# Kernel optimization log

Measured on AMD Instinct MI355X. Metric: run time of the kernel, lower is better.

Reference implementation:

```python
import jax, jax.numpy as jnp
import numpy as np

B, L, H = 32, 2048, 1024

def setup_inputs() -> dict:
    key = jax.random.key(0)
    ks = jax.random.split(key, 10)
    scale = 1.0 / np.sqrt(H)
    return {
        "query": jax.random.normal(ks[0], (B, 1, H), dtype=jnp.float32),
        "key": jax.random.normal(ks[1], (B, L, H), dtype=jnp.float32),
        "value": jax.random.normal(ks[2], (B, L, H), dtype=jnp.float32),
        "mask": jax.random.randint(ks[3], (B, L), 0, 2, dtype=jnp.int32),
        "Wa_w": jax.random.normal(ks[4], (H, H), dtype=jnp.float32) * scale,
        "Wa_b": jax.random.normal(ks[5], (H,), dtype=jnp.float32) * scale,
        "Ua_w": jax.random.normal(ks[6], (H, H), dtype=jnp.float32) * scale,
        "Ua_b": jax.random.normal(ks[7], (H,), dtype=jnp.float32) * scale,
        "va_w": jax.random.normal(ks[8], (1, H), dtype=jnp.float32) * scale,
        "va_b": jax.random.normal(ks[9], (1,), dtype=jnp.float32) * scale,
    }

def reference(query, key, value, mask, Wa_w, Wa_b, Ua_w, Ua_b, va_w, va_b):
    # query: [B,1,H] -> squeeze, project with Wa
    q = jnp.einsum('bh,oh->bo', query[:, 0, :], Wa_w) + Wa_b          # [B,H]
    # key: [B,L,H] projected with Ua
    k = jnp.einsum('blh,oh->blo', key, Ua_w) + Ua_b                   # [B,L,H]
    # additive score: va . tanh(Wa q + Ua h)
    s = jnp.tanh(q[:, None, :] + k)                                    # [B,L,H]
    score = jnp.einsum('blh,h->bl', s, va_w[0]) + va_b[0]             # [B,L]
    score = jnp.where(mask == 0, jnp.float32(-1e10), score)
    attn = jax.nn.softmax(score, axis=1)                               # [B,L]
    context = jnp.einsum('bl,blh->bh', attn, value)[:, None, :]       # [B,1,H]
    return context
```

## Files before the change

kernel.cpp:

```cpp
#include <hip/hip_runtime.h>
#include <hip/hip_bf16.h>


#define B_ 32
#define L_ 2048
#define H_ 1024

typedef __attribute__((ext_vector_type(8))) short bf16x8;
typedef __attribute__((ext_vector_type(16))) float f32x16;
typedef __attribute__((ext_vector_type(4))) float f32x4;

__device__ inline unsigned pk_bf16(float a, float b) {
    unsigned r;
    asm("v_cvt_pk_bf16_f32 %0, %1, %2" : "=v"(r) : "v"(a), "v"(b));
    return r;
}

__device__ inline float fast_tanh(float x) {
    float e = __expf(2.f * x);
    return 1.f - 2.f * __builtin_amdgcn_rcpf(e + 1.f);
}

__device__ inline f32x4 ntload4(const float* p) {
    return __builtin_nontemporal_load((const f32x4*)p);
}

__device__ inline int aslot(int s, int m, int lf) {
    return (((s * 2 + m) * 64) + (lf ^ (s & 7))) * 8;
}

__global__ void prep_ua(const float* __restrict__ Ua, ushort* __restrict__ Ufrag) {
    int t = blockIdx.x * 256 + threadIdx.x;
    int lane = t & 63;
    int nb   = (t >> 6) & 31;
    int s    = t >> 11;
    int o = nb * 32 + (lane & 31);
    int h = s * 16 + (lane >> 5) * 8;
    const float* src = Ua + o * H_ + h;
    f32x4 f0 = *(const f32x4*)(src);
    f32x4 f1 = *(const f32x4*)(src + 4);
    uint4 pk;
    pk.x = pk_bf16(f0.x, f0.y);
    pk.y = pk_bf16(f0.z, f0.w);
    pk.z = pk_bf16(f1.x, f1.y);
    pk.w = pk_bf16(f1.z, f1.w);
    *(uint4*)(Ufrag + (size_t)t * 8) = pk;
}

__global__ void prep_q(const float* __restrict__ query, const float* __restrict__ Wa_w,
                       const float* __restrict__ Wa_b, const float* __restrict__ Ua_b,
                       float* __restrict__ qbuf) {
    int wid  = blockIdx.x * 4 + (threadIdx.x >> 6);
    int lane = threadIdx.x & 63;
    int b = wid >> 10, o = wid & 1023;
    const float* qrow = query + b * H_;
    const float* wrow = Wa_w + o * H_;
    float acc = 0.f;
    #pragma unroll
    for (int i = 0; i < 16; ++i) {
        int h = i * 64 + lane;
        acc += qrow[h] * wrow[h];
    }
    #pragma unroll
    for (int m = 1; m < 64; m <<= 1) acc += __shfl_xor(acc, m);
    if (lane == 0) qbuf[b * H_ + o] = acc + Wa_b[o] + Ua_b[o];
}

__launch_bounds__(1024, 4)
__global__ void score_kernel(const float* __restrict__ key, const ushort* __restrict__ Ufrag,
                             const float* __restrict__ qbuf, const float* __restrict__ va_w,
                             const float* __restrict__ va_b, const int* __restrict__ mask,
                             float* __restrict__ scorebuf) {
    __shared__ ushort Alds[2][16384];
    __shared__ float s_part[16][64];

    int bid = blockIdx.x;
    int b = bid >> 5, lt = bid & 31;
    int l0 = lt * 64;
    int tid = threadIdx.x;
    int w = tid >> 6, lane = tid & 63;

    int r    = tid >> 4;
    int c0s  = tid & 15;
    int c0   = c0s * 16;
    int mblk = r >> 5;
    int rr   = r & 31;
    const float* krow = key + ((size_t)b * L_ + (l0 + r)) * H_;

    int nb0 = w * 2;
    const ushort* Uw = Ufrag + ((size_t)nb0 * 64 + lane) * 8;

    f32x4 ld[4];
    #pragma unroll
    for (int i = 0; i < 4; ++i) ld[i] = ntload4(krow + c0 + 4 * i);
    bf16x8 bc[2], b1[2];
    #pragma unroll
    for (int ni = 0; ni < 2; ++ni) {
        bc[ni] = *(const bf16x8*)(Uw + ni * 512);
        b1[ni] = *(const bf16x8*)(Uw + (size_t)16384 + ni * 512);
    }
    {
        uint4 pk0, pk1;
        pk0.x = pk_bf16(ld[0].x, ld[0].y);
        pk0.y = pk_bf16(ld[0].z, ld[0].w);
        pk0.z = pk_bf16(ld[1].x, ld[1].y);
        pk0.w = pk_bf16(ld[1].z, ld[1].w);
        pk1.x = pk_bf16(ld[2].x, ld[2].y);
        pk1.y = pk_bf16(ld[2].z, ld[2].w);
        pk1.z = pk_bf16(ld[3].x, ld[3].y);
        pk1.w = pk_bf16(ld[3].z, ld[3].w);
        *(uint4*)&Alds[0][aslot(c0s, mblk, rr)]      = pk0;
        *(uint4*)&Alds[0][aslot(c0s, mblk, 32 + rr)] = pk1;
    }
    __syncthreads();

    f32x16 acc[2][2] = {};

    for (int kc = 0; kc < 4; ++kc) {
        int cur = kc & 1;
        if (kc < 3) {
            #pragma unroll
            for (int i = 0; i < 4; ++i)
                ld[i] = ntload4(krow + (kc + 1) * 256 + c0 + 4 * i);
        }
        #pragma unroll 4
        for (int s = 0; s < 16; ++s) {
            bf16x8 a0 = *(const bf16x8*)&Alds[cur][aslot(s, 0, lane)];
            bf16x8 a1 = *(const bf16x8*)&Alds[cur][aslot(s, 1, lane)];
            int gp = (kc * 16 + s + 2) & 63;
            bf16x8 bn0 = *(const bf16x8*)(Uw + (size_t)gp * 16384);
            bf16x8 bn1 = *(const bf16x8*)(Uw + (size_t)gp * 16384 + 512);
            acc[0][0] = __builtin_amdgcn_mfma_f32_32x32x16_bf16(a0, bc[0], acc[0][0], 0, 0, 0);
            acc[1][0] = __builtin_amdgcn_mfma_f32_32x32x16_bf16(a1, bc[0], acc[1][0], 0, 0, 0);
            acc[0][1] = __builtin_amdgcn_mfma_f32_32x32x16_bf16(a0, bc[1], acc[0][1], 0, 0, 0);
            acc[1][1] = __builtin_amdgcn_mfma_f32_32x32x16_bf16(a1, bc[1], acc[1][1], 0, 0, 0);
            bc[0] = b1[0]; bc[1] = b1[1];
            b1[0] = bn0;   b1[1] = bn1;
        }
        if (kc < 3) {
            uint4 pk0, pk1;
            pk0.x = pk_bf16(ld[0].x, ld[0].y);
            pk0.y = pk_bf16(ld[0].z, ld[0].w);
            pk0.z = pk_bf16(ld[1].x, ld[1].y);
            pk0.w = pk_bf16(ld[1].z, ld[1].w);
            pk1.x = pk_bf16(ld[2].x, ld[2].y);
            pk1.y = pk_bf16(ld[2].z, ld[2].w);
            pk1.z = pk_bf16(ld[3].x, ld[3].y);
            pk1.w = pk_bf16(ld[3].z, ld[3].w);
            *(uint4*)&Alds[cur ^ 1][aslot(c0s, mblk, rr)]      = pk0;
            *(uint4*)&Alds[cur ^ 1][aslot(c0s, mblk, 32 + rr)] = pk1;
            __syncthreads();
        }
    }

    #pragma unroll
    for (int mi = 0; mi < 2; ++mi) {
        float rowsum[16];
        #pragma unroll
        for (int rg = 0; rg < 16; ++rg) rowsum[rg] = 0.f;
        #pragma unroll
        for (int ni = 0; ni < 2; ++ni) {
            int col = w * 64 + ni * 32 + (lane & 31);
            float qv  = qbuf[b * H_ + col];
            float vav = va_w[col];
            #pragma unroll
            for (int rg = 0; rg < 16; ++rg)
                rowsum[rg] += vav * fast_tanh(qv + acc[mi][ni][rg]);
        }
        #pragma unroll
        for (int rg = 0; rg < 16; ++rg) {
            float v = rowsum[rg];
            v += __shfl_xor(v, 1);  v += __shfl_xor(v, 2);  v += __shfl_xor(v, 4);
            v += __shfl_xor(v, 8);  v += __shfl_xor(v, 16);
            if ((lane & 31) == 0) {
                int row = mi * 32 + (rg & 3) + 8 * (rg >> 2) + 4 * (lane >> 5);
                s_part[w][row] = v;
            }
        }
    }
    __syncthreads();
    if (tid < 64) {
        float s = 0.f;
        #pragma unroll
        for (int ww = 0; ww < 16; ++ww) s += s_part[ww][tid];
        int l = l0 + tid;
        int m = mask[b * L_ + l];
        scorebuf[b * L_ + l] = (m == 0) ? -1e10f : (s + va_b[0]);
    }
}

__global__ void softmax_kernel(const float* __restrict__ scorebuf, float* __restrict__ attn) {
    __shared__ float red[16];
    int b = blockIdx.x;
    int tid = threadIdx.x;
    float v[8];
    float mx = -3e38f;
    #pragma unroll
    for (int i = 0; i < 8; ++i) {
        v[i] = scorebuf[b * L_ + tid + i * 256];
        mx = fmaxf(mx, v[i]);
    }
    #pragma unroll
    for (int m = 1; m < 64; m <<= 1) mx = fmaxf(mx, __shfl_xor(mx, m));
    if ((tid & 63) == 0) red[tid >> 6] = mx;
    __syncthreads();
    mx = fmaxf(fmaxf(red[0], red[1]), fmaxf(red[2], red[3]));
    float sum = 0.f;
    #pragma unroll
    for (int i = 0; i < 8; ++i) { v[i] = __expf(v[i] - mx); sum += v[i]; }
    #pragma unroll
    for (int m = 1; m < 64; m <<= 1) sum += __shfl_xor(sum, m);
    if ((tid & 63) == 0) red[8 + (tid >> 6)] = sum;
    __syncthreads();
    sum = red[8] + red[9] + red[10] + red[11];
    float inv = 1.f / sum;
    #pragma unroll
    for (int i = 0; i < 8; ++i) attn[b * L_ + tid + i * 256] = v[i] * inv;
}

__global__ void context_kernel(const float* __restrict__ attn, const float* __restrict__ value,
                               float* __restrict__ partial) {
    int bid = blockIdx.x;
    int b = bid >> 4, ch = bid & 15;
    int l0 = ch * 128;
    int tid = threadIdx.x;
    f32x4 acc = {0.f, 0.f, 0.f, 0.f};
    const float* vbase = value + ((size_t)b * L_ + l0) * H_ + tid * 4;
    const float* arow  = attn + b * L_ + l0;
    for (int l = 0; l < 128; ++l) {
        float a = arow[l];
        f32x4 vv = *(const f32x4*)(vbase + (size_t)l * H_);
        acc.x += a * vv.x; acc.y += a * vv.y; acc.z += a * vv.z; acc.w += a * vv.w;
    }
    *(f32x4*)(partial + (size_t)bid * H_ + tid * 4) = acc;
}

__global__ void reduce_kernel(const float* __restrict__ partial, float* __restrict__ out) {
    int t = blockIdx.x * 256 + threadIdx.x;
    int b = t >> 10, h = t & 1023;
    float s = 0.f;
    #pragma unroll
    for (int c = 0; c < 16; ++c) s += partial[(size_t)(b * 16 + c) * H_ + h];
    out[t] = s;
}

extern "C" void kernel_launch(void* const* d_in, const int* in_sizes, int n_in,
                              void* d_out, int out_size, void* d_ws, size_t ws_size,
                              hipStream_t stream) {
    const float* query = (const float*)d_in[0];
    const float* key   = (const float*)d_in[1];
    const float* value = (const float*)d_in[2];
    const int*   mask  = (const int*)d_in[3];
    const float* Wa_w  = (const float*)d_in[4];
    const float* Wa_b  = (const float*)d_in[5];
    const float* Ua_w  = (const float*)d_in[6];
    const float* Ua_b  = (const float*)d_in[7];
    const float* va_w  = (const float*)d_in[8];
    const float* va_b  = (const float*)d_in[9];
    float* out = (float*)d_out;

    char* ws = (char*)d_ws;
    ushort* Ufrag    = (ushort*)ws;
    float*  qbuf     = (float*)(ws + (2u << 20));
    float*  scorebuf = (float*)(ws + (2u << 20) + (128u << 10));
    float*  attnb    = (float*)(ws + (2u << 20) + (384u << 10));
    float*  partial  = (float*)(ws + (2u << 20) + (640u << 10));

    hipLaunchKernelGGL(prep_ua,        dim3(512),  dim3(256),  0, stream, Ua_w, Ufrag);
    hipLaunchKernelGGL(prep_q,         dim3(8192), dim3(256),  0, stream, query, Wa_w, Wa_b, Ua_b, qbuf);
    hipLaunchKernelGGL(score_kernel,   dim3(1024), dim3(1024), 0, stream, key, Ufrag, qbuf, va_w, va_b, mask, scorebuf);
    hipLaunchKernelGGL(softmax_kernel, dim3(32),   dim3(256),  0, stream, scorebuf, attnb);
    hipLaunchKernelGGL(context_kernel, dim3(512),  dim3(256),  0, stream, attnb, value, partial);
    hipLaunchKernelGGL(reduce_kernel,  dim3(128),  dim3(256),  0, stream, partial, out);
}
```

Before: 275.4 us.

## Interleave key prefetch and LDS staging into MFMA loop with per-step barriers

```diff
diff --git a/kernel.cpp b/kernel.cpp
--- a/kernel.cpp
+++ b/kernel.cpp
@@ -93,12 +93,11 @@
     f32x4 ld[4];
     #pragma unroll
     for (int i = 0; i < 4; ++i) ld[i] = ntload4(krow + c0 + 4 * i);
-    bf16x8 bc[2], b1[2];
-    #pragma unroll
-    for (int ni = 0; ni < 2; ++ni) {
-        bc[ni] = *(const bf16x8*)(Uw + ni * 512);
-        b1[ni] = *(const bf16x8*)(Uw + (size_t)16384 + ni * 512);
-    }
+    bf16x8 bc0, bc1, bn0, bn1;
+    bc0 = *(const bf16x8*)(Uw);
+    bc1 = *(const bf16x8*)(Uw + 512);
+    bn0 = *(const bf16x8*)(Uw + (size_t)16384);
+    bn1 = *(const bf16x8*)(Uw + (size_t)16384 + 512);
     {
         uint4 pk0, pk1;
         pk0.x = pk_bf16(ld[0].x, ld[0].y);
@@ -112,44 +111,56 @@
         *(uint4*)&Alds[0][aslot(c0s, mblk, rr)]      = pk0;
         *(uint4*)&Alds[0][aslot(c0s, mblk, 32 + rr)] = pk1;
     }
-    __syncthreads();
+    asm volatile("s_waitcnt lgkmcnt(0)" ::: "memory");
+    __builtin_amdgcn_s_barrier();
 
     f32x16 acc[2][2] = {};
 
+    #pragma unroll 1
     for (int kc = 0; kc < 4; ++kc) {
         int cur = kc & 1;
-        if (kc < 3) {
-            #pragma unroll
-            for (int i = 0; i < 4; ++i)
-                ld[i] = ntload4(krow + (kc + 1) * 256 + c0 + 4 * i);
-        }
-        #pragma unroll 4
+        bool notlast = (kc < 3);
+        #pragma unroll
         for (int s = 0; s < 16; ++s) {
             bf16x8 a0 = *(const bf16x8*)&Alds[cur][aslot(s, 0, lane)];
             bf16x8 a1 = *(const bf16x8*)&Alds[cur][aslot(s, 1, lane)];
             int gp = (kc * 16 + s + 2) & 63;
-            bf16x8 bn0 = *(const bf16x8*)(Uw + (size_t)gp * 16384);
-            bf16x8 bn1 = *(const bf16x8*)(Uw + (size_t)gp * 16384 + 512);
-            acc[0][0] = __builtin_amdgcn_mfma_f32_32x32x16_bf16(a0, bc[0], acc[0][0], 0, 0, 0);
-            acc[1][0] = __builtin_amdgcn_mfma_f32_32x32x16_bf16(a1, bc[0], acc[1][0], 0, 0, 0);
-            acc[0][1] = __builtin_amdgcn_mfma_f32_32x32x16_bf16(a0, bc[1], acc[0][1], 0, 0, 0);
-            acc[1][1] = __builtin_amdgcn_mfma_f32_32x32x16_bf16(a1, bc[1], acc[1][1], 0, 0, 0);
-            bc[0] = b1[0]; bc[1] = b1[1];
-            b1[0] = bn0;   b1[1] = bn1;
-        }
-        if (kc < 3) {
-            uint4 pk0, pk1;
-            pk0.x = pk_bf16(ld[0].x, ld[0].y);
-            pk0.y = pk_bf16(ld[0].z, ld[0].w);
-            pk0.z = pk_bf16(ld[1].x, ld[1].y);
-            pk0.w = pk_bf16(ld[1].z, ld[1].w);
-            pk1.x = pk_bf16(ld[2].x, ld[2].y);
-            pk1.y = pk_bf16(ld[2].z, ld[2].w);
-            pk1.z = pk_bf16(ld[3].x, ld[3].y);
-            pk1.w = pk_bf16(ld[3].z, ld[3].w);
-            *(uint4*)&Alds[cur ^ 1][aslot(c0s, mblk, rr)]      = pk0;
-            *(uint4*)&Alds[cur ^ 1][aslot(c0s, mblk, 32 + rr)] = pk1;
-            __syncthreads();
+            bf16x8 bt0 = *(const bf16x8*)(Uw + (size_t)gp * 16384);
+            bf16x8 bt1 = *(const bf16x8*)(Uw + (size_t)gp * 16384 + 512);
+            if (notlast && s < 4)
+                ld[s] = ntload4(krow + (kc + 1) * 256 + c0 + 4 * s);
+
+            __builtin_amdgcn_s_barrier();
+            asm volatile("s_waitcnt lgkmcnt(0)" ::: "memory");
+            __builtin_amdgcn_sched_barrier(0);
+            __builtin_amdgcn_s_setprio(1);
+            acc[0][0] = __builtin_amdgcn_mfma_f32_32x32x16_bf16(a0, bc0, acc[0][0], 0, 0, 0);
+            acc[1][0] = __builtin_amdgcn_mfma_f32_32x32x16_bf16(a1, bc0, acc[1][0], 0, 0, 0);
+            acc[0][1] = __builtin_amdgcn_mfma_f32_32x32x16_bf16(a0, bc1, acc[0][1], 0, 0, 0);
+            acc[1][1] = __builtin_amdgcn_mfma_f32_32x32x16_bf16(a1, bc1, acc[1][1], 0, 0, 0);
+            __builtin_amdgcn_s_setprio(0);
+            bc0 = bn0; bc1 = bn1;
+            bn0 = bt0; bn1 = bt1;
+
+            if (notlast && s == 12) {
+                uint4 pk0;
+                pk0.x = pk_bf16(ld[0].x, ld[0].y);
+                pk0.y = pk_bf16(ld[0].z, ld[0].w);
+                pk0.z = pk_bf16(ld[1].x, ld[1].y);
+                pk0.w = pk_bf16(ld[1].z, ld[1].w);
+                *(uint4*)&Alds[cur ^ 1][aslot(c0s, mblk, rr)] = pk0;
+                asm volatile("s_waitcnt lgkmcnt(0)" ::: "memory");
+            }
+            if (notlast && s == 13) {
+                uint4 pk1;
+                pk1.x = pk_bf16(ld[2].x, ld[2].y);
+                pk1.y = pk_bf16(ld[2].z, ld[2].w);
+                pk1.z = pk_bf16(ld[3].x, ld[3].y);
+                pk1.w = pk_bf16(ld[3].z, ld[3].w);
+                *(uint4*)&Alds[cur ^ 1][aslot(c0s, mblk, 32 + rr)] = pk1;
+                asm volatile("s_waitcnt lgkmcnt(0)" ::: "memory");
+            }
+            __builtin_amdgcn_s_barrier();
         }
     }
 
```

After: 357.0 us. +29.6%, slower.
